# Optimization experiments

Hardware: AMD Instinct MI355X
Metric: run time of the kernel (lower is better)

## Reference

```python
import jax, jax.numpy as jnp
import numpy as np
from jax import lax

B, T, D, H = 64, 2048, 256, 256


def setup_inputs() -> dict:
    key = jax.random.key(0)
    k1, k2, k3 = jax.random.split(key, 3)
    xs = jax.random.normal(k1, (B, T, D), dtype=jnp.float32)
    # scale weights ~ 1/sqrt(fan_in) to keep tanh out of saturation
    W_ih = jax.random.normal(k2, (D, H), dtype=jnp.float32) / np.sqrt(D)
    W_hh = jax.random.normal(k3, (H, H), dtype=jnp.float32) / np.sqrt(H)
    b_hh = jnp.zeros((H,), dtype=jnp.float32)
    c = jnp.zeros((B, H), dtype=jnp.float32)
    return {"c": c, "xs": xs, "W_ih": W_ih, "W_hh": W_hh, "b_hh": b_hh}


def reference(c, xs, W_ih, W_hh, b_hh):
    # Elman RNN: h_t = tanh(x_t @ W_ih + h_{t-1} @ W_hh + b_hh)
    # (the ih bias is created but never applied in the original module)
    # Precompute the input projection for all timesteps in one big GEMM.
    px = jnp.einsum('btd,dh->bth', xs, W_ih)  # [B, T, H]

    def step(h, px_t):
        h_new = jnp.tanh(h @ W_hh + b_hh + px_t)
        return h_new, h_new

    h_final, ys = lax.scan(step, c, px.transpose(1, 0, 2))  # ys: [T, B, H]
    return h_final, ys.transpose(1, 0, 2)  # carry [B,H], outputs [B,T,H]
```

## Files before the change

### kernel.cpp

```cpp
#include <hip/hip_runtime.h>


typedef _Float16 half8 __attribute__((ext_vector_type(8)));
typedef float floatx4 __attribute__((ext_vector_type(4)));
typedef float f32x4 __attribute__((ext_vector_type(4)));

constexpr int Bb = 64, Tt = 2048, Dd = 256, Hh = 256;

__device__ __forceinline__ int lds_addr(int row, int col) {
    return row * 512 + ((((col >> 3) ^ (row & 7)) & 31) << 4) + ((col & 7) << 1);
}

__device__ __forceinline__ float fast_tanh(float x) {
    float e = __builtin_amdgcn_exp2f(x * 2.885390081777927f);
    float r = __builtin_amdgcn_rcpf(e + 1.0f);
    return __builtin_fmaf(-2.0f, r, 1.0f);
}

__global__ __launch_bounds__(256, 2) void px_gemm(const float* __restrict__ xs,
                                                  const float* __restrict__ Wih,
                                                  const float* __restrict__ bhh,
                                                  float* __restrict__ px) {
    const int lane = threadIdx.x & 63;
    const int w = threadIdx.x >> 6;
    const int q = lane >> 4;
    const int m = lane & 15;

    half8 bf[4][8];
#pragma unroll
    for (int tt = 0; tt < 4; ++tt) {
        const int n = 64 * w + 16 * tt + m;
#pragma unroll
        for (int c = 0; c < 8; ++c) {
            half8 f;
#pragma unroll
            for (int j = 0; j < 8; ++j)
                f[j] = (_Float16)Wih[(32 * c + 8 * q + j) * Hh + n];
            bf[tt][c] = f;
        }
    }
    float bias[4];
#pragma unroll
    for (int tt = 0; tt < 4; ++tt) bias[tt] = bhh[64 * w + 16 * tt + m];

    for (int i = 0; i < 8; ++i) {
        const int tau = blockIdx.x * 8 + i;
        const float* arow = xs + (size_t)(tau * 16 + m) * Dd;
        half8 af[8];
#pragma unroll
        for (int c = 0; c < 8; ++c) {
            f32x4 lo = *(const f32x4*)(arow + 32 * c + 8 * q);
            f32x4 hi = *(const f32x4*)(arow + 32 * c + 8 * q + 4);
            half8 f;
            f[0] = (_Float16)lo[0]; f[1] = (_Float16)lo[1];
            f[2] = (_Float16)lo[2]; f[3] = (_Float16)lo[3];
            f[4] = (_Float16)hi[0]; f[5] = (_Float16)hi[1];
            f[6] = (_Float16)hi[2]; f[7] = (_Float16)hi[3];
            af[c] = f;
        }
        floatx4 acc[4];
#pragma unroll
        for (int tt = 0; tt < 4; ++tt) {
            acc[tt][0] = bias[tt]; acc[tt][1] = bias[tt];
            acc[tt][2] = bias[tt]; acc[tt][3] = bias[tt];
        }
#pragma unroll
        for (int c = 0; c < 8; ++c)
#pragma unroll
            for (int tt = 0; tt < 4; ++tt)
                acc[tt] = __builtin_amdgcn_mfma_f32_16x16x32_f16(af[c], bf[tt][c], acc[tt], 0, 0, 0);
#pragma unroll
        for (int tt = 0; tt < 4; ++tt)
#pragma unroll
            for (int r = 0; r < 4; ++r)
                px[(size_t)(tau * 16 + 4 * q + r) * Hh + 64 * w + 16 * tt + m] = acc[tt][r];
    }
}

__global__ __launch_bounds__(512, 1) void rnn_scan(const float* __restrict__ c0,
                                                   const float* __restrict__ Whh,
                                                   float* __restrict__ hfin,
                                                   float* __restrict__ ys) {
    __shared__ alignas(16) unsigned char hb[2][8192];
    const int g = blockIdx.x;
    const int lane = threadIdx.x & 63;
    const int w = threadIdx.x >> 6;
    const int q = lane >> 4;
    const int m = lane & 15;

    half8 bf[2][8];
#pragma unroll
    for (int tt = 0; tt < 2; ++tt) {
        const int n = 32 * w + 16 * tt + m;
#pragma unroll
        for (int c = 0; c < 8; ++c) {
            half8 f;
#pragma unroll
            for (int j = 0; j < 8; ++j)
                f[j] = (_Float16)Whh[(32 * c + 8 * q + j) * Hh + n];
            bf[tt][c] = f;
        }
    }

    for (int i = threadIdx.x; i < 16 * 256; i += 512) {
        const int row = i >> 8, col = i & 255;
        *(_Float16*)&hb[0][lds_addr(row, col)] = (_Float16)c0[(16 * g + row) * Hh + col];
    }

    size_t rowoff[4];
#pragma unroll
    for (int r = 0; r < 4; ++r)
        rowoff[r] = (size_t)(16 * g + 4 * q + r) * Tt * Hh;
    int coloff[2];
    coloff[0] = 32 * w + m;
    coloff[1] = 32 * w + 16 + m;

    float pxc[8], pxn[8];
#pragma unroll
    for (int tt = 0; tt < 2; ++tt)
#pragma unroll
        for (int r = 0; r < 4; ++r)
            pxc[4 * tt + r] = ys[rowoff[r] + coloff[tt]];

    __syncthreads();

    for (int t = 0; t < Tt; ++t) {
        const int p = t & 1;
        const int tn = (t + 1 < Tt) ? t + 1 : t;
#pragma unroll
        for (int tt = 0; tt < 2; ++tt)
#pragma unroll
            for (int r = 0; r < 4; ++r)
                pxn[4 * tt + r] = ys[rowoff[r] + (size_t)tn * Hh + coloff[tt]];

        half8 af[8];
#pragma unroll
        for (int c = 0; c < 8; ++c)
            af[c] = *(const half8*)&hb[p][m * 512 + ((((4 * c + q) ^ (m & 7)) & 31) << 4)];

        floatx4 acc[2];
#pragma unroll
        for (int tt = 0; tt < 2; ++tt) {
            acc[tt][0] = pxc[4 * tt + 0]; acc[tt][1] = pxc[4 * tt + 1];
            acc[tt][2] = pxc[4 * tt + 2]; acc[tt][3] = pxc[4 * tt + 3];
        }
#pragma unroll
        for (int tt = 0; tt < 2; ++tt)
#pragma unroll
            for (int c = 0; c < 8; ++c)
                acc[tt] = __builtin_amdgcn_mfma_f32_16x16x32_f16(af[c], bf[tt][c], acc[tt], 0, 0, 0);

#pragma unroll
        for (int tt = 0; tt < 2; ++tt) {
#pragma unroll
            for (int r = 0; r < 4; ++r) {
                const float h = fast_tanh(acc[tt][r]);
                const int row = 4 * q + r;
                const int col = coloff[tt];
                ys[rowoff[r] + (size_t)t * Hh + col] = h;
                *(_Float16*)&hb[p ^ 1][lds_addr(row, col)] = (_Float16)h;
                if (t == Tt - 1) hfin[(16 * g + row) * Hh + col] = h;
            }
        }
#pragma unroll
        for (int k = 0; k < 8; ++k) pxc[k] = pxn[k];
        __syncthreads();
    }
}

extern "C" void kernel_launch(void* const* d_in, const int* in_sizes, int n_in,
                              void* d_out, int out_size, void* d_ws, size_t ws_size,
                              hipStream_t stream) {
    const float* c0  = (const float*)d_in[0];
    const float* xs  = (const float*)d_in[1];
    const float* Wih = (const float*)d_in[2];
    const float* Whh = (const float*)d_in[3];
    const float* bhh = (const float*)d_in[4];
    float* out = (float*)d_out;
    float* hfin = out;
    float* ys = out + Bb * Hh;

    px_gemm<<<1024, 256, 0, stream>>>(xs, Wih, bhh, ys);
    rnn_scan<<<Bb / 16, 512, 0, stream>>>(c0, Whh, hfin, ys);
}
```

Baseline: 1.764 ms.

## Use 4 waves per scan block, unroll timesteps by two, prefetch px two steps ahead

The recurrent scan kernel drops from 8 to 4 waves per block, with each wave computing 64 hidden columns (4 MFMA tiles), which halves the number of waves at each per-step barrier. The time loop is unrolled by two with fixed LDS ping-pong buffers and precomputed LDS read and write addresses. Pointer arithmetic replaces the size_t offset recomputation, and px loads for step t+2 are issued after the first MFMA to hide their latency. The LDS swizzle adds a row&8 term to reduce bank conflicts. The trade-off is more registers per wave and less wave-level parallelism for hiding latency.

```diff
diff --git a/kernel.cpp b/kernel.cpp
--- a/kernel.cpp
+++ b/kernel.cpp
@@ -8,7 +8,8 @@
 constexpr int Bb = 64, Tt = 2048, Dd = 256, Hh = 256;
 
 __device__ __forceinline__ int lds_addr(int row, int col) {
-    return row * 512 + ((((col >> 3) ^ (row & 7)) & 31) << 4) + ((col & 7) << 1);
+    const int blk = ((col >> 3) ^ (row & 7) ^ (row & 8)) & 31;
+    return row * 512 + (blk << 4) + ((col & 7) << 1);
 }
 
 __device__ __forceinline__ float fast_tanh(float x) {
@@ -77,21 +78,22 @@
     }
 }
 
-__global__ __launch_bounds__(512, 1) void rnn_scan(const float* __restrict__ c0,
+__global__ __launch_bounds__(256, 1) void rnn_scan(const float* __restrict__ c0,
                                                    const float* __restrict__ Whh,
                                                    float* __restrict__ hfin,
                                                    float* __restrict__ ys) {
     __shared__ alignas(16) unsigned char hb[2][8192];
+    char* const L = (char*)&hb[0][0];
     const int g = blockIdx.x;
     const int lane = threadIdx.x & 63;
     const int w = threadIdx.x >> 6;
     const int q = lane >> 4;
     const int m = lane & 15;
 
-    half8 bf[2][8];
-#pragma unroll
-    for (int tt = 0; tt < 2; ++tt) {
-        const int n = 32 * w + 16 * tt + m;
+    half8 bf[4][8];
+#pragma unroll
+    for (int tt = 0; tt < 4; ++tt) {
+        const int n = 64 * w + 16 * tt + m;
 #pragma unroll
         for (int c = 0; c < 8; ++c) {
             half8 f;
@@ -102,69 +104,108 @@
         }
     }
 
-    for (int i = threadIdx.x; i < 16 * 256; i += 512) {
+    for (int i = threadIdx.x; i < 16 * 256; i += 256) {
         const int row = i >> 8, col = i & 255;
-        *(_Float16*)&hb[0][lds_addr(row, col)] = (_Float16)c0[(16 * g + row) * Hh + col];
-    }
-
-    size_t rowoff[4];
+        *(_Float16*)&L[lds_addr(row, col)] = (_Float16)c0[(16 * g + row) * Hh + col];
+    }
+
+    int ra[8];
+#pragma unroll
+    for (int c = 0; c < 8; ++c)
+        ra[c] = m * 512 + (((((4 * c + q)) ^ (m & 7) ^ (m & 8)) & 31) << 4);
+    int wa[16];
+#pragma unroll
+    for (int tt = 0; tt < 4; ++tt)
+#pragma unroll
+        for (int r = 0; r < 4; ++r)
+            wa[4 * tt + r] = lds_addr(4 * q + r, 64 * w + 16 * tt + m);
+
+    const float* pr[4];
 #pragma unroll
     for (int r = 0; r < 4; ++r)
-        rowoff[r] = (size_t)(16 * g + 4 * q + r) * Tt * Hh;
-    int coloff[2];
-    coloff[0] = 32 * w + m;
-    coloff[1] = 32 * w + 16 + m;
-
-    float pxc[8], pxn[8];
-#pragma unroll
-    for (int tt = 0; tt < 2; ++tt)
-#pragma unroll
-        for (int r = 0; r < 4; ++r)
-            pxc[4 * tt + r] = ys[rowoff[r] + coloff[tt]];
+        pr[r] = ys + (size_t)(16 * g + 4 * q + r) * Tt * Hh + 64 * w + m;
+
+    floatx4 s0[4], s1[4];
+#pragma unroll
+    for (int tt = 0; tt < 4; ++tt)
+#pragma unroll
+        for (int r = 0; r < 4; ++r) {
+            s0[tt][r] = pr[r][16 * tt];
+            s1[tt][r] = pr[r][256 + 16 * tt];
+        }
+#pragma unroll
+    for (int r = 0; r < 4; ++r) pr[r] += 512;
 
     __syncthreads();
 
-    for (int t = 0; t < Tt; ++t) {
-        const int p = t & 1;
-        const int tn = (t + 1 < Tt) ? t + 1 : t;
-#pragma unroll
-        for (int tt = 0; tt < 2; ++tt)
-#pragma unroll
-            for (int r = 0; r < 4; ++r)
-                pxn[4 * tt + r] = ys[rowoff[r] + (size_t)tn * Hh + coloff[tt]];
-
-        half8 af[8];
-#pragma unroll
-        for (int c = 0; c < 8; ++c)
-            af[c] = *(const half8*)&hb[p][m * 512 + ((((4 * c + q) ^ (m & 7)) & 31) << 4)];
-
-        floatx4 acc[2];
-#pragma unroll
-        for (int tt = 0; tt < 2; ++tt) {
-            acc[tt][0] = pxc[4 * tt + 0]; acc[tt][1] = pxc[4 * tt + 1];
-            acc[tt][2] = pxc[4 * tt + 2]; acc[tt][3] = pxc[4 * tt + 3];
-        }
-#pragma unroll
-        for (int tt = 0; tt < 2; ++tt)
+    for (int t = 0; t < Tt; t += 2) {
+        {
+            half8 af[8];
 #pragma unroll
             for (int c = 0; c < 8; ++c)
-                acc[tt] = __builtin_amdgcn_mfma_f32_16x16x32_f16(af[c], bf[tt][c], acc[tt], 0, 0, 0);
-
-#pragma unroll
-        for (int tt = 0; tt < 2; ++tt) {
-#pragma unroll
-            for (int r = 0; r < 4; ++r) {
-                const float h = fast_tanh(acc[tt][r]);
-                const int row = 4 * q + r;
-                const int col = coloff[tt];
-                ys[rowoff[r] + (size_t)t * Hh + col] = h;
-                *(_Float16*)&hb[p ^ 1][lds_addr(row, col)] = (_Float16)h;
-                if (t == Tt - 1) hfin[(16 * g + row) * Hh + col] = h;
+                af[c] = *(const half8*)(L + ra[c]);
+            floatx4 acc[4];
+#pragma unroll
+            for (int tt = 0; tt < 4; ++tt)
+                acc[tt] = __builtin_amdgcn_mfma_f32_16x16x32_f16(af[0], bf[tt][0], s0[tt], 0, 0, 0);
+            if (t + 2 < Tt) {
+#pragma unroll
+                for (int tt = 0; tt < 4; ++tt)
+#pragma unroll
+                    for (int r = 0; r < 4; ++r)
+                        s0[tt][r] = pr[r][16 * tt];
             }
-        }
-#pragma unroll
-        for (int k = 0; k < 8; ++k) pxc[k] = pxn[k];
-        __syncthreads();
+#pragma unroll
+            for (int c = 1; c < 8; ++c)
+#pragma unroll
+                for (int tt = 0; tt < 4; ++tt)
+                    acc[tt] = __builtin_amdgcn_mfma_f32_16x16x32_f16(af[c], bf[tt][c], acc[tt], 0, 0, 0);
+#pragma unroll
+            for (int tt = 0; tt < 4; ++tt)
+#pragma unroll
+                for (int r = 0; r < 4; ++r) {
+                    const float h = fast_tanh(acc[tt][r]);
+                    ((float*)pr[r])[16 * tt - 512] = h;
+                    *(_Float16*)(L + 8192 + wa[4 * tt + r]) = (_Float16)h;
+                }
+            __syncthreads();
+        }
+        {
+            half8 af[8];
+#pragma unroll
+            for (int c = 0; c < 8; ++c)
+                af[c] = *(const half8*)(L + 8192 + ra[c]);
+            floatx4 acc[4];
+#pragma unroll
+            for (int tt = 0; tt < 4; ++tt)
+                acc[tt] = __builtin_amdgcn_mfma_f32_16x16x32_f16(af[0], bf[tt][0], s1[tt], 0, 0, 0);
+            if (t + 3 < Tt) {
+#pragma unroll
+                for (int tt = 0; tt < 4; ++tt)
+#pragma unroll
+                    for (int r = 0; r < 4; ++r)
+                        s1[tt][r] = pr[r][256 + 16 * tt];
+            }
+#pragma unroll
+            for (int c = 1; c < 8; ++c)
+#pragma unroll
+                for (int tt = 0; tt < 4; ++tt)
+                    acc[tt] = __builtin_amdgcn_mfma_f32_16x16x32_f16(af[c], bf[tt][c], acc[tt], 0, 0, 0);
+            const bool last = (t + 2 == Tt);
+#pragma unroll
+            for (int tt = 0; tt < 4; ++tt)
+#pragma unroll
+                for (int r = 0; r < 4; ++r) {
+                    const float h = fast_tanh(acc[tt][r]);
+                    ((float*)pr[r])[16 * tt - 256] = h;
+                    *(_Float16*)(L + wa[4 * tt + r]) = (_Float16)h;
+                    if (last)
+                        hfin[(16 * g + 4 * q + r) * Hh + 64 * w + 16 * tt + m] = h;
+                }
+#pragma unroll
+            for (int r = 0; r < 4; ++r) pr[r] += 512;
+            __syncthreads();
+        }
     }
 }
 
@@ -181,5 +222,5 @@
     float* ys = out + Bb * Hh;
 
     px_gemm<<<1024, 256, 0, stream>>>(xs, Wih, bhh, ys);
-    rnn_scan<<<Bb / 16, 512, 0, stream>>>(c0, Whh, hfin, ys);
-}
+    rnn_scan<<<Bb / 16, 256, 0, stream>>>(c0, Whh, hfin, ys);
+}
```

Result: slower. 2.669 ms (+51.3%).
